# Kernel optimization log

Hardware: AMD Instinct MI355X
Metric: run time of the kernel (lower is better)

Reference implementation:

```python
import jax, jax.numpy as jnp
import numpy as np

T, D = 4096, 1024
S = 32768
DIST_DIM = 20
BINS = jnp.array([1, 2, 3, 4, 8, 16, 32, 64], dtype=jnp.int64)


def setup_inputs() -> dict:
    key = jax.random.key(0)
    ks = jax.random.split(key, 16)
    scale = 1.0 / np.sqrt(D)
    inp = {
        "embeds": jax.random.normal(ks[0], (T, D), dtype=jnp.float32),
        "states": jax.random.normal(ks[1], (T, D), dtype=jnp.float32),
        # MHA (1 head) projection params, torch Linear convention: x @ W.T + b
        "Wq": jax.random.normal(ks[2], (D, D), dtype=jnp.float32) * scale,
        "bq": jnp.zeros((D,), dtype=jnp.float32),
        "Wk": jax.random.normal(ks[3], (D, D), dtype=jnp.float32) * scale,
        "bk": jnp.zeros((D,), dtype=jnp.float32),
        "Wv": jax.random.normal(ks[4], (D, D), dtype=jnp.float32) * scale,
        "bv": jnp.zeros((D,), dtype=jnp.float32),
        "Wo": jax.random.normal(ks[5], (D, D), dtype=jnp.float32) * scale,
        "bo": jnp.zeros((D,), dtype=jnp.float32),
        # distance embedding table: len(bins)+1 = 9 rows
        "dist_embed": jax.random.normal(ks[6], (9, DIST_DIM), dtype=jnp.float32),
        "span_starts": jax.random.randint(ks[7], (S,), 0, T - 30, dtype=jnp.int64),
        "span_lengths": jax.random.randint(ks[8], (S,), 0, 30, dtype=jnp.int64),
    }
    return inp


def reference(embeds, states, Wq, bq, Wk, bk, Wv, bv, Wo, bo, dist_embed,
              span_starts, span_lengths):
    d = states.shape[1]
    # Single-head attention: query=states, key=states, value=embeds (seq len T, batch 1)
    q = states @ Wq.T + bq                      # [T, D]
    k = states @ Wk.T + bk                      # [T, D]
    v = embeds @ Wv.T + bv                      # [T, D]
    scores = (q @ k.T) / jnp.sqrt(jnp.asarray(d, q.dtype))   # [T, T]
    attn = jax.nn.softmax(scores, axis=-1)
    attn_embeds = (attn @ v) @ Wo.T + bo        # [T, D]

    ends = span_starts + span_lengths           # inclusive end, width 1..30
    # ragged per-span segment sum over [start, end] via prefix sums
    cs = jnp.concatenate([jnp.zeros((1, d), attn_embeds.dtype),
                          jnp.cumsum(attn_embeds, axis=0)], axis=0)  # [T+1, D]
    span_sum = cs[ends + 1] - cs[span_starts]   # [S, D]

    span_start_end = jnp.concatenate([states[span_starts], states[ends]], axis=1)  # [S, 2D]

    lengths = span_lengths + 1                  # len(span) = end - start + 1
    bin_idx = jnp.sum(lengths[:, None] > BINS[None, :], axis=-1)  # [S] in [0, 8]
    len_embed = dist_embed[bin_idx]             # [S, DIST_DIM] (dropout omitted: eval mode)

    return jnp.concatenate([span_sum, span_start_end, len_embed], axis=1)  # [S, 3D+20]
```

## Files before the change

kernel.cpp:

```cpp
#include <hip/hip_runtime.h>
#include <hip/hip_bf16.h>


typedef __attribute__((ext_vector_type(8))) short bf16x8;
typedef __attribute__((ext_vector_type(4))) short bf16x4;
typedef __attribute__((ext_vector_type(4))) float f32x4;

#define T_DIM 4096
#define D_DIM 1024
#define S_NUM 32768

#define GLOBAL_LOAD_LDS16(gptr, ldsptr)                                        \
  __builtin_amdgcn_global_load_lds(                                            \
      (const __attribute__((address_space(1))) void*)(gptr),                   \
      (__attribute__((address_space(3))) void*)(ldsptr), 16, 0, 0)

__global__ __launch_bounds__(256) void cast2_bf16(const float* __restrict__ a,
                                                  const float* __restrict__ b,
                                                  __hip_bfloat16* __restrict__ oa,
                                                  __hip_bfloat16* __restrict__ ob) {
  const float* s = blockIdx.z ? b : a;
  __hip_bfloat16* d = blockIdx.z ? ob : oa;
  int i = blockIdx.x * 256 + threadIdx.x;
  float2 v = ((const float2*)s)[i];
  __hip_bfloat162 o;
  o.x = __float2bfloat16(v.x);
  o.y = __float2bfloat16(v.y);
  ((__hip_bfloat162*)d)[i] = o;
}

__global__ __launch_bounds__(256) void cast1_bf16(const float* __restrict__ a,
                                                  __hip_bfloat16* __restrict__ oa) {
  int i = blockIdx.x * 256 + threadIdx.x;
  float2 v = ((const float2*)a)[i];
  __hip_bfloat162 o;
  o.x = __float2bfloat16(v.x);
  o.y = __float2bfloat16(v.y);
  ((__hip_bfloat162*)oa)[i] = o;
}

__global__ __launch_bounds__(256) void transpose_cast_bf16(const float* __restrict__ wq,
                                                           const float* __restrict__ wk,
                                                           const float* __restrict__ wv,
                                                           __hip_bfloat16* __restrict__ oq,
                                                           __hip_bfloat16* __restrict__ ok,
                                                           __hip_bfloat16* __restrict__ ov) {
  __shared__ float tile[64][65];
  const int z = blockIdx.z;
  const float* in = z == 0 ? wq : z == 1 ? wk : wv;
  __hip_bfloat16* out = z == 0 ? oq : z == 1 ? ok : ov;
  const int bx = blockIdx.x * 64;
  const int by = blockIdx.y * 64;
  const int t = threadIdx.x;
  const int r = t >> 4;
  const int c4 = (t & 15) * 4;
#pragma unroll
  for (int p = 0; p < 4; p++) {
    const float4 v = *(const float4*)&in[(size_t)(by + p * 16 + r) * D_DIM + bx + c4];
    tile[p * 16 + r][c4] = v.x;
    tile[p * 16 + r][c4 + 1] = v.y;
    tile[p * 16 + r][c4 + 2] = v.z;
    tile[p * 16 + r][c4 + 3] = v.w;
  }
  __syncthreads();
#pragma unroll
  for (int p = 0; p < 4; p++) {
    const int orow = p * 16 + r;
    bf16x4 o4;
#pragma unroll
    for (int q = 0; q < 4; q++) {
      __hip_bfloat16 h = __float2bfloat16(tile[c4 + q][orow]);
      o4[q] = *reinterpret_cast<short*>(&h);
    }
    *reinterpret_cast<bf16x4*>(&out[(size_t)(bx + orow) * D_DIM + by + c4]) = o4;
  }
}

__global__ __launch_bounds__(256) void zero_f32(float* __restrict__ p, int n) {
  int i = blockIdx.x * 256 + threadIdx.x;
  if (i < n) p[i] = 0.0f;
}

__global__ __launch_bounds__(256) void hvec(const float* __restrict__ Wo,
                                            const float* __restrict__ bv,
                                            const float* __restrict__ bo,
                                            const __hip_bfloat16* __restrict__ WqT,
                                            const __hip_bfloat16* __restrict__ WkT,
                                            const float* __restrict__ bq,
                                            const float* __restrict__ bk,
                                            float* __restrict__ bvo,
                                            float* __restrict__ h1,
                                            float* __restrict__ h2,
                                            float* __restrict__ c0) {
  const int z = blockIdx.z;
  const int wave = threadIdx.x >> 6, lane = threadIdx.x & 63;
  const int row = blockIdx.x * 4 + wave;
  if (z == 3 && (blockIdx.x != 0 || wave != 0)) return;
  float s = 0.0f;
  if (z == 0) {
    for (int k2 = lane; k2 < D_DIM; k2 += 64) s += Wo[(size_t)row * D_DIM + k2] * bv[k2];
  } else if (z == 1) {
    for (int k2 = lane; k2 < D_DIM; k2 += 64)
      s += __bfloat162float(WqT[(size_t)row * D_DIM + k2]) * bk[k2];
  } else if (z == 2) {
    for (int k2 = lane; k2 < D_DIM; k2 += 64)
      s += __bfloat162float(WkT[(size_t)row * D_DIM + k2]) * bq[k2];
  } else {
    for (int k2 = lane; k2 < D_DIM; k2 += 64) s += bq[k2] * bk[k2];
  }
#pragma unroll
  for (int off = 32; off; off >>= 1) s += __shfl_xor(s, off);
  if (lane == 0) {
    if (z == 0) bvo[row] = s + bo[row];
    else if (z == 1) h1[row] = s;
    else if (z == 2) h2[row] = s;
    else c0[0] = s;
  }
}

__global__ __launch_bounds__(256) void uw_vec(const float* __restrict__ states,
                                              const float* __restrict__ h1,
                                              const float* __restrict__ h2,
                                              const float* __restrict__ c0,
                                              float* __restrict__ u,
                                              float* __restrict__ w) {
  const int z = blockIdx.z;
  const int wave = threadIdx.x >> 6, lane = threadIdx.x & 63;
  const int row = blockIdx.x * 4 + wave;
  const float* h = z == 0 ? h1 : h2;
  float s = 0.0f;
  for (int k2 = lane; k2 < D_DIM; k2 += 64) s += states[(size_t)row * D_DIM + k2] * h[k2];
#pragma unroll
  for (int off = 32; off; off >>= 1) s += __shfl_xor(s, off);
  if (lane == 0) {
    if (z == 0) u[row] = s + c0[0];
    else w[row] = s;
  }
}

__device__ __forceinline__ void gemm_core_128(const __hip_bfloat16* __restrict__ A,
                                              const __hip_bfloat16* __restrict__ B,
                                              int K, int lda, int ldb,
                                              int bm, int bn,
                                              __hip_bfloat16* As,
                                              __hip_bfloat16* Bs,
                                              f32x4 acc[4][4]) {
  const int tid = threadIdx.x;
  const int wave = tid >> 6, lane = tid & 63;
  const int srow = lane >> 2, scol = (lane & 3) * 8;
  const __hip_bfloat16* Ag0 = A + (size_t)(bm + wave * 16 + srow) * lda + scol;
  const __hip_bfloat16* Ag1 = Ag0 + (size_t)64 * lda;
  const __hip_bfloat16* Bg0 = B + (size_t)(bn + wave * 16 + srow) * ldb + scol;
  const __hip_bfloat16* Bg1 = Bg0 + (size_t)64 * ldb;
  const int c0 = wave * 512, c1 = (4 + wave) * 512;
  const int wtr = (wave >> 1) * 64, wtc = (wave & 1) * 64;
  const int lr = lane & 15, lk = (lane >> 4) * 8;

  GLOBAL_LOAD_LDS16(Ag0, As + c0);
  GLOBAL_LOAD_LDS16(Ag1, As + c1);
  GLOBAL_LOAD_LDS16(Bg0, Bs + c0);
  GLOBAL_LOAD_LDS16(Bg1, Bs + c1);

  int cur = 0;
  for (int k0 = 0; k0 < K; k0 += 32) {
    __syncthreads();
    const int nxt = cur ^ 1;
    if (k0 + 32 < K) {
      const int kn = k0 + 32;
      GLOBAL_LOAD_LDS16(Ag0 + kn, As + nxt * 4096 + c0);
      GLOBAL_LOAD_LDS16(Ag1 + kn, As + nxt * 4096 + c1);
      GLOBAL_LOAD_LDS16(Bg0 + kn, Bs + nxt * 4096 + c0);
      GLOBAL_LOAD_LDS16(Bg1 + kn, Bs + nxt * 4096 + c1);
    }
    const __hip_bfloat16* a = As + cur * 4096;
    const __hip_bfloat16* b = Bs + cur * 4096;
    bf16x8 af[4], bfr[4];
#pragma unroll
    for (int i = 0; i < 4; i++)
      af[i] = *(const bf16x8*)&a[(wtr + i * 16 + lr) * 32 + lk];
#pragma unroll
    for (int j = 0; j < 4; j++)
      bfr[j] = *(const bf16x8*)&b[(wtc + j * 16 + lr) * 32 + lk];
#pragma unroll
    for (int i = 0; i < 4; i++)
#pragma unroll
      for (int j = 0; j < 4; j++)
        acc[i][j] = __builtin_amdgcn_mfma_f32_16x16x32_bf16(af[i], bfr[j], acc[i][j], 0, 0, 0);
    cur = nxt;
  }
}


__global__ __launch_bounds__(256) void small_gemm_splitk(const __hip_bfloat16* __restrict__ Wo_bf,
                                                         const __hip_bfloat16* __restrict__ WvT_bf,
                                                         const __hip_bfloat16* __restrict__ WkT_bf,
                                                         const __hip_bfloat16* __restrict__ WqT_bf,
                                                         float* __restrict__ part) {
  __shared__ __hip_bfloat16 As[2 * 128 * 32];
  __shared__ __hip_bfloat16 Bs[2 * 128 * 32];
  const int z = blockIdx.z;
  const int zz = z & 3;
  const __hip_bfloat16* A = (z < 4) ? Wo_bf + zz * 256 : WkT_bf + zz * 256;
  const __hip_bfloat16* B = (z < 4) ? WvT_bf + zz * 256 : WqT_bf + zz * 256;
  const int bm = blockIdx.y * 128, bn = blockIdx.x * 128;
  const int wave = threadIdx.x >> 6, lane = threadIdx.x & 63;
  const int wtr = (wave >> 1) * 64, wtc = (wave & 1) * 64;
  const int lr = lane & 15;
  f32x4 acc[4][4] = {};
  gemm_core_128(A, B, 256, D_DIM, D_DIM, bm, bn, As, Bs, acc);
  float* dst = part + (size_t)z * D_DIM * D_DIM;
#pragma unroll
  for (int j = 0; j < 4; j++) {
    const int col = bn + wtc + j * 16 + lr;
#pragma unroll
    for (int i = 0; i < 4; i++)
#pragma unroll
      for (int r = 0; r < 4; r++) {
        const int row = bm + wtr + i * 16 + (lane >> 4) * 4 + r;
        dst[(size_t)row * D_DIM + col] = acc[i][j][r];
      }
  }
}

__global__ __launch_bounds__(256) void small_combine(const float* __restrict__ part,
                                                     __hip_bfloat16* __restrict__ wvo,
                                                     __hip_bfloat16* __restrict__ m1) {
  const size_t idx = (size_t)blockIdx.x * 256 + threadIdx.x;
  const size_t n = (size_t)D_DIM * D_DIM / 4;
  const f32x4* base = (const f32x4*)part + (size_t)blockIdx.z * 4 * n;
  f32x4 s = base[idx] + base[idx + n] + base[idx + 2 * n] + base[idx + 3 * n];
  bf16x4 o;
#pragma unroll
  for (int q = 0; q < 4; q++) {
    __hip_bfloat16 h = __float2bfloat16(s[q]);
    o[q] = *reinterpret_cast<short*>(&h);
  }
  __hip_bfloat16* out = blockIdx.z == 0 ? wvo : m1;
  ((bf16x4*)out)[idx] = o;
}

__global__ __launch_bounds__(256) void proj_gemm(const __hip_bfloat16* __restrict__ states_bf,
                                                 const __hip_bfloat16* __restrict__ embeds_bf,
                                                 const __hip_bfloat16* __restrict__ M1,
                                                 const __hip_bfloat16* __restrict__ Wvo,
                                                 __hip_bfloat16* __restrict__ tmp,
                                                 __hip_bfloat16* __restrict__ vT) {
  __shared__ __hip_bfloat16 As[2 * 128 * 32];
  __shared__ __hip_bfloat16 Bs[2 * 128 * 32];
  const int z = blockIdx.z;
  const __hip_bfloat16* A = (z == 0) ? states_bf : embeds_bf;
  const __hip_bfloat16* B = (z == 0) ? M1 : Wvo;
  const int bm = blockIdx.y * 128, bn = blockIdx.x * 128;
  const int wave = threadIdx.x >> 6, lane = threadIdx.x & 63;
  const int wtr = (wave >> 1) * 64, wtc = (wave & 1) * 64;
  const int lr = lane & 15;
  f32x4 acc[4][4] = {};
  gemm_core_128(A, B, D_DIM, D_DIM, D_DIM, bm, bn, As, Bs, acc);

#pragma unroll
  for (int j = 0; j < 4; j++) {
    const int col = bn + wtc + j * 16 + lr;
#pragma unroll
    for (int i = 0; i < 4; i++) {
#pragma unroll
      for (int r = 0; r < 4; r++) {
        const int row = bm + wtr + i * 16 + (lane >> 4) * 4 + r;
        const __hip_bfloat16 val = __float2bfloat16(acc[i][j][r]);
        if (z == 0)
          tmp[(size_t)row * D_DIM + col] = val;
        else
          vT[(size_t)col * T_DIM + row] = val;
      }
    }
  }
}

__global__ __launch_bounds__(256) void scoresP_gemm(const __hip_bfloat16* __restrict__ tmp,
                                                    const __hip_bfloat16* __restrict__ states_bf,
                                                    const float* __restrict__ u,
                                                    const float* __restrict__ w,
                                                    __hip_bfloat16* __restrict__ P,
                                                    float* __restrict__ l) {
  __shared__ __hip_bfloat16 As[2 * 128 * 32];
  __shared__ __hip_bfloat16 Bs[2 * 128 * 32];
  const int bm = blockIdx.y * 128, bn = blockIdx.x * 128;
  const int wave = threadIdx.x >> 6, lane = threadIdx.x & 63;
  const int wtr = (wave >> 1) * 64, wtc = (wave & 1) * 64;
  const int lr = lane & 15;
  f32x4 acc[4][4] = {};
  gemm_core_128(tmp, states_bf, D_DIM, D_DIM, D_DIM, bm, bn, As, Bs, acc);

  float rowsum[4][4];
#pragma unroll
  for (int i = 0; i < 4; i++)
#pragma unroll
    for (int r = 0; r < 4; r++) rowsum[i][r] = 0.0f;

#pragma unroll
  for (int j = 0; j < 4; j++) {
    const int col = bn + wtc + j * 16 + lr;
    const float ww = w[col];
#pragma unroll
    for (int i = 0; i < 4; i++) {
#pragma unroll
      for (int r = 0; r < 4; r++) {
        const int row = bm + wtr + i * 16 + (lane >> 4) * 4 + r;
        const float e = __expf((acc[i][j][r] + u[row] + ww) * 0.03125f);
        P[(size_t)row * T_DIM + col] = __float2bfloat16(e);
        rowsum[i][r] += e;
      }
    }
  }
#pragma unroll
  for (int off = 1; off < 16; off <<= 1)
#pragma unroll
    for (int i = 0; i < 4; i++)
#pragma unroll
      for (int r = 0; r < 4; r++)
        rowsum[i][r] += __shfl_xor(rowsum[i][r], off);
  if ((lane & 15) == 0) {
#pragma unroll
    for (int i = 0; i < 4; i++)
#pragma unroll
      for (int r = 0; r < 4; r++) {
        const int row = bm + wtr + i * 16 + (lane >> 4) * 4 + r;
        atomicAdd(&l[row], rowsum[i][r]);
      }
  }
}

__global__ __launch_bounds__(256) void pv_gemm_splitk(const __hip_bfloat16* __restrict__ P,
                                                      const __hip_bfloat16* __restrict__ vT,
                                                      float* __restrict__ part) {
  __shared__ __hip_bfloat16 As[2 * 128 * 32];
  __shared__ __hip_bfloat16 Bs[2 * 128 * 32];
  const int z = blockIdx.z;
  const int bm = blockIdx.y * 128, bn = blockIdx.x * 128;
  const int wave = threadIdx.x >> 6, lane = threadIdx.x & 63;
  const int wtr = (wave >> 1) * 64, wtc = (wave & 1) * 64;
  const int lr = lane & 15;
  f32x4 acc[4][4] = {};
  gemm_core_128(P + z * 2048, vT + z * 2048, 2048, T_DIM, T_DIM, bm, bn, As, Bs, acc);
  float* dst = part + (size_t)z * T_DIM * D_DIM;
#pragma unroll
  for (int j = 0; j < 4; j++) {
    const int col = bn + wtc + j * 16 + lr;
#pragma unroll
    for (int i = 0; i < 4; i++)
#pragma unroll
      for (int r = 0; r < 4; r++) {
        const int row = bm + wtr + i * 16 + (lane >> 4) * 4 + r;
        dst[(size_t)row * D_DIM + col] = acc[i][j][r];
      }
  }
}

__global__ __launch_bounds__(256) void pv_combine_colsum(const float* __restrict__ part,
                                                         const float* __restrict__ l,
                                                         const float* __restrict__ bvo,
                                                         float* __restrict__ ao,
                                                         float* __restrict__ partT) {
  const int col = blockIdx.x * 256 + threadIdx.x;
  const int ch = blockIdx.y;
  const size_t n = (size_t)T_DIM * D_DIM;
  const float bb = bvo[col];
  float s = 0.0f;
  for (int i = 0; i < 64; i++) {
    const int row = ch * 64 + i;
    const float inv = 1.0f / l[row];
    const size_t idx = (size_t)row * D_DIM + col;
    const float v = (part[idx] + part[n + idx]) * inv + bb;
    ao[idx] = v;
    s += v;
  }
  partT[(col << 6) | ch] = s;
}

__global__ __launch_bounds__(256) void write_cs(const float* __restrict__ x,
                                                const float* __restrict__ partT,
                                                float* __restrict__ cs) {
  const int col = blockIdx.x * 256 + threadIdx.x;
  const int ch = blockIdx.y;
  float run = 0.0f;
  for (int c = 0; c < ch; c++) run += partT[(col << 6) | c];
  if (ch == 0) cs[col] = 0.0f;
  const float* p = x + (size_t)ch * 64 * D_DIM + col;
  float* q = cs + ((size_t)(ch * 64 + 1)) * D_DIM + col;
  for (int i = 0; i < 64; i++) {
    run += p[i * D_DIM];
    q[i * D_DIM] = run;
  }
}

__global__ __launch_bounds__(256) void hist_k(const int* __restrict__ starts,
                                              int* __restrict__ hist) {
  const int s = blockIdx.x * 256 + threadIdx.x;
  atomicAdd(&hist[starts[s]], 1);
}

__global__ __launch_bounds__(1024) void scan_hist(const int* __restrict__ hist,
                                                  int* __restrict__ offs) {
  __shared__ int sums[1024];
  const int t = threadIdx.x;
  const int v0 = hist[t * 4], v1 = hist[t * 4 + 1];
  const int v2 = hist[t * 4 + 2], v3 = hist[t * 4 + 3];
  const int tot = v0 + v1 + v2 + v3;
  sums[t] = tot;
  __syncthreads();
  for (int off = 1; off < 1024; off <<= 1) {
    const int x = (t >= off) ? sums[t - off] : 0;
    __syncthreads();
    sums[t] += x;
    __syncthreads();
  }
  const int excl = sums[t] - tot;
  offs[t * 4] = excl;
  offs[t * 4 + 1] = excl + v0;
  offs[t * 4 + 2] = excl + v0 + v1;
  offs[t * 4 + 3] = excl + v0 + v1 + v2;
}

__global__ __launch_bounds__(256) void scatter_k(const int* __restrict__ starts,
                                                 int* __restrict__ offs,
                                                 int* __restrict__ perm) {
  const int s = blockIdx.x * 256 + threadIdx.x;
  const int pos = atomicAdd(&offs[starts[s]], 1);
  perm[pos] = s;
}

__global__ __launch_bounds__(256) void span_gather(const float* __restrict__ cs,
                                                   const float* __restrict__ states,
                                                   const float* __restrict__ dist,
                                                   const int* __restrict__ starts,
                                                   const int* __restrict__ lens,
                                                   const int* __restrict__ perm,
                                                   float* __restrict__ out) {
  const int s = perm[blockIdx.x];
  const int start = starts[s];
  const int len = lens[s];
  const int end = start + len;
  const int length = len + 1;
  const int bin = (length > 1) + (length > 2) + (length > 3) + (length > 4) +
                  (length > 8) + (length > 16) + (length > 32) + (length > 64);
  const f32x4* csS = (const f32x4*)(cs + (size_t)start * D_DIM);
  const f32x4* csE = (const f32x4*)(cs + (size_t)(end + 1) * D_DIM);
  const f32x4* stS = (const f32x4*)(states + (size_t)start * D_DIM);
  const f32x4* stE = (const f32x4*)(states + (size_t)end * D_DIM);
  const f32x4* de = (const f32x4*)(dist + bin * 20);
  f32x4* o = (f32x4*)(out + (size_t)s * 3092);
  for (int j = threadIdx.x; j < 773; j += 256) {
    f32x4 r;
    if (j < 256) {
      r = csE[j] - csS[j];
    } else if (j < 512) {
      r = stS[j - 256];
    } else if (j < 768) {
      r = stE[j - 512];
    } else {
      r = de[j - 768];
    }
    __builtin_nontemporal_store(r, o + j);
  }
}

extern "C" void kernel_launch(void* const* d_in, const int* in_sizes, int n_in,
                              void* d_out, int out_size, void* d_ws, size_t ws_size,
                              hipStream_t stream) {
  const float* embeds = (const float*)d_in[0];
  const float* states = (const float*)d_in[1];
  const float* Wq = (const float*)d_in[2];
  const float* bq = (const float*)d_in[3];
  const float* Wk = (const float*)d_in[4];
  const float* bk = (const float*)d_in[5];
  const float* Wv = (const float*)d_in[6];
  const float* bv = (const float*)d_in[7];
  const float* Wo = (const float*)d_in[8];
  const float* bo = (const float*)d_in[9];
  const float* dist = (const float*)d_in[10];
  const int* starts = (const int*)d_in[11];
  const int* lens = (const int*)d_in[12];
  float* out = (float*)d_out;

  const size_t TD = (size_t)T_DIM * D_DIM;
  const size_t DD = (size_t)D_DIM * D_DIM;
  const size_t TT = (size_t)T_DIM * T_DIM;

  char* w = (char*)d_ws;
  size_t off = 0;
  auto alloc = [&](size_t bytes) {
    char* p = w + off;
    off = (off + bytes + 255) & ~(size_t)255;
    return p;
  };
  __hip_bfloat16* states_bf = (__hip_bfloat16*)alloc(TD * 2);
  __hip_bfloat16* embeds_bf = (__hip_bfloat16*)alloc(TD * 2);
  __hip_bfloat16* Wo_bf = (__hip_bfloat16*)alloc(DD * 2);
  __hip_bfloat16* WqT_bf = (__hip_bfloat16*)alloc(DD * 2);
  __hip_bfloat16* WkT_bf = (__hip_bfloat16*)alloc(DD * 2);
  __hip_bfloat16* WvT_bf = (__hip_bfloat16*)alloc(DD * 2);
  __hip_bfloat16* Wvo_bf = (__hip_bfloat16*)alloc(DD * 2);
  __hip_bfloat16* M1_bf = (__hip_bfloat16*)alloc(DD * 2);
  __hip_bfloat16* tmp_bf = (__hip_bfloat16*)alloc(TD * 2);
  __hip_bfloat16* vT_bf = (__hip_bfloat16*)alloc(TD * 2);
  __hip_bfloat16* P_bf = (__hip_bfloat16*)alloc(TT * 2);
  float* l_sum = (float*)alloc(T_DIM * 4);
  int* hist = (int*)alloc(T_DIM * 4);
  int* offs = (int*)alloc(T_DIM * 4);
  int* perm = (int*)alloc(S_NUM * 4);
  float* bvo = (float*)alloc(D_DIM * 4);
  float* h1 = (float*)alloc(D_DIM * 4);
  float* h2 = (float*)alloc(D_DIM * 4);
  float* c0 = (float*)alloc(256);
  float* u = (float*)alloc(T_DIM * 4);
  float* wv_ = (float*)alloc(T_DIM * 4);
  float* ao = (float*)alloc(TD * 4);
  float* cs = (float*)alloc((size_t)(T_DIM + 1) * D_DIM * 4);
  float* partT = (float*)alloc(64 * D_DIM * 4);
  float* wpart = (float*)alloc(8 * DD * 4);
  float* pv_part = (float*)alloc(2 * TD * 4);
  if (off > ws_size) return;

  cast2_bf16<<<dim3(TD / 512, 1, 2), 256, 0, stream>>>(states, embeds, states_bf, embeds_bf);
  cast1_bf16<<<DD / 512, 256, 0, stream>>>(Wo, Wo_bf);
  transpose_cast_bf16<<<dim3(16, 16, 3), 256, 0, stream>>>(Wq, Wk, Wv, WqT_bf, WkT_bf, WvT_bf);
  zero_f32<<<2 * T_DIM / 256, 256, 0, stream>>>(l_sum, 2 * T_DIM);
  hvec<<<dim3(D_DIM / 4, 1, 4), 256, 0, stream>>>(Wo, bv, bo, WqT_bf, WkT_bf, bq, bk,
                                                  bvo, h1, h2, c0);

  hist_k<<<S_NUM / 256, 256, 0, stream>>>(starts, hist);
  scan_hist<<<1, 1024, 0, stream>>>(hist, offs);
  scatter_k<<<S_NUM / 256, 256, 0, stream>>>(starts, offs, perm);

  uw_vec<<<dim3(T_DIM / 4, 1, 2), 256, 0, stream>>>(states, h1, h2, c0, u, wv_);

  small_gemm_splitk<<<dim3(D_DIM / 128, D_DIM / 128, 8), 256, 0, stream>>>(
      Wo_bf, WvT_bf, WkT_bf, WqT_bf, wpart);
  small_combine<<<dim3(DD / 1024, 1, 2), 256, 0, stream>>>(wpart, Wvo_bf, M1_bf);

  proj_gemm<<<dim3(D_DIM / 128, T_DIM / 128, 2), 256, 0, stream>>>(
      states_bf, embeds_bf, M1_bf, Wvo_bf, tmp_bf, vT_bf);

  scoresP_gemm<<<dim3(T_DIM / 128, T_DIM / 128), 256, 0, stream>>>(
      tmp_bf, states_bf, u, wv_, P_bf, l_sum);

  pv_gemm_splitk<<<dim3(D_DIM / 128, T_DIM / 128, 2), 256, 0, stream>>>(P_bf, vT_bf, pv_part);
  pv_combine_colsum<<<dim3(4, 64), 256, 0, stream>>>(pv_part, l_sum, bvo, ao, partT);

  write_cs<<<dim3(4, 64), 256, 0, stream>>>(ao, partT, cs);

  span_gather<<<S_NUM, 256, 0, stream>>>(cs, states, dist, starts, lens, perm, out);
}
```

Baseline: 725.9 us.

## Replace split-K PV GEMM with 128x64 tiles and fused normalize/colsum epilogue

Drops split-K in the P·V GEMM and shrinks the N tile to 64 so the grid keeps the same block count, giving each block the full K range. The softmax normalization, bias add, ao write and per-64-row column partial sums now happen in the GEMM epilogue via wave shuffles. This removes the separate combine kernel and the write and read of two fp32 T×D partial buffers. The cost is a longer K loop per block and less B-tile reuse per A load.

Measured after the change: 726.6 us. About the same (+0.1%).

```diff
diff --git a/kernel.cpp b/kernel.cpp
--- a/kernel.cpp
+++ b/kernel.cpp
@@ -190,6 +190,55 @@
   }
 }
 
+__device__ __forceinline__ void gemm_core_128x64(const __hip_bfloat16* __restrict__ A,
+                                                 const __hip_bfloat16* __restrict__ B,
+                                                 int K, int lda, int ldb,
+                                                 int bm, int bn,
+                                                 __hip_bfloat16* As,
+                                                 __hip_bfloat16* Bs,
+                                                 f32x4 acc[4][2]) {
+  const int tid = threadIdx.x;
+  const int wave = tid >> 6, lane = tid & 63;
+  const int srow = lane >> 2, scol = (lane & 3) * 8;
+  const __hip_bfloat16* Ag0 = A + (size_t)(bm + wave * 16 + srow) * lda + scol;
+  const __hip_bfloat16* Ag1 = Ag0 + (size_t)64 * lda;
+  const __hip_bfloat16* Bg0 = B + (size_t)(bn + wave * 16 + srow) * ldb + scol;
+  const int c0 = wave * 512, c1 = (4 + wave) * 512;
+  const int wtr = (wave >> 1) * 64, wtc = (wave & 1) * 32;
+  const int lr = lane & 15, lk = (lane >> 4) * 8;
+
+  GLOBAL_LOAD_LDS16(Ag0, As + c0);
+  GLOBAL_LOAD_LDS16(Ag1, As + c1);
+  GLOBAL_LOAD_LDS16(Bg0, Bs + c0);
+
+  int cur = 0;
+  for (int k0 = 0; k0 < K; k0 += 32) {
+    __syncthreads();
+    const int nxt = cur ^ 1;
+    if (k0 + 32 < K) {
+      const int kn = k0 + 32;
+      GLOBAL_LOAD_LDS16(Ag0 + kn, As + nxt * 4096 + c0);
+      GLOBAL_LOAD_LDS16(Ag1 + kn, As + nxt * 4096 + c1);
+      GLOBAL_LOAD_LDS16(Bg0 + kn, Bs + nxt * 2048 + c0);
+    }
+    const __hip_bfloat16* a = As + cur * 4096;
+    const __hip_bfloat16* b = Bs + cur * 2048;
+    bf16x8 af[4], bfr[2];
+#pragma unroll
+    for (int i = 0; i < 4; i++)
+      af[i] = *(const bf16x8*)&a[(wtr + i * 16 + lr) * 32 + lk];
+#pragma unroll
+    for (int j = 0; j < 2; j++)
+      bfr[j] = *(const bf16x8*)&b[(wtc + j * 16 + lr) * 32 + lk];
+#pragma unroll
+    for (int i = 0; i < 4; i++)
+#pragma unroll
+      for (int j = 0; j < 2; j++)
+        acc[i][j] = __builtin_amdgcn_mfma_f32_16x16x32_bf16(af[i], bfr[j], acc[i][j], 0, 0, 0);
+    cur = nxt;
+  }
+}
+
 
 __global__ __launch_bounds__(256) void small_gemm_splitk(const __hip_bfloat16* __restrict__ Wo_bf,
                                                          const __hip_bfloat16* __restrict__ WvT_bf,
@@ -329,51 +378,59 @@
   }
 }
 
-__global__ __launch_bounds__(256) void pv_gemm_splitk(const __hip_bfloat16* __restrict__ P,
-                                                      const __hip_bfloat16* __restrict__ vT,
-                                                      float* __restrict__ part) {
+__global__ __launch_bounds__(256) void pv_gemm(const __hip_bfloat16* __restrict__ P,
+                                               const __hip_bfloat16* __restrict__ vT,
+                                               const float* __restrict__ l,
+                                               const float* __restrict__ bvo,
+                                               float* __restrict__ ao,
+                                               float* __restrict__ partT) {
   __shared__ __hip_bfloat16 As[2 * 128 * 32];
-  __shared__ __hip_bfloat16 Bs[2 * 128 * 32];
-  const int z = blockIdx.z;
-  const int bm = blockIdx.y * 128, bn = blockIdx.x * 128;
+  __shared__ __hip_bfloat16 Bs[2 * 64 * 32];
+  const int bm = blockIdx.y * 128, bn = blockIdx.x * 64;
   const int wave = threadIdx.x >> 6, lane = threadIdx.x & 63;
-  const int wtr = (wave >> 1) * 64, wtc = (wave & 1) * 64;
+  const int wtr = (wave >> 1) * 64, wtc = (wave & 1) * 32;
   const int lr = lane & 15;
-  f32x4 acc[4][4] = {};
-  gemm_core_128(P + z * 2048, vT + z * 2048, 2048, T_DIM, T_DIM, bm, bn, As, Bs, acc);
-  float* dst = part + (size_t)z * T_DIM * D_DIM;
-#pragma unroll
-  for (int j = 0; j < 4; j++) {
+  f32x4 acc[4][2] = {};
+  gemm_core_128x64(P, vT, T_DIM, T_DIM, T_DIM, bm, bn, As, Bs, acc);
+
+  float inv[4][4];
+#pragma unroll
+  for (int i = 0; i < 4; i++)
+#pragma unroll
+    for (int r = 0; r < 4; r++) {
+      const int row = bm + wtr + i * 16 + (lane >> 4) * 4 + r;
+      inv[i][r] = 1.0f / l[row];
+    }
+  const int ch = (bm >> 6) + (wave >> 1);
+  float csum[2];
+#pragma unroll
+  for (int j = 0; j < 2; j++) {
     const int col = bn + wtc + j * 16 + lr;
+    const float bb = bvo[col];
+    float s = 0.0f;
 #pragma unroll
     for (int i = 0; i < 4; i++)
 #pragma unroll
       for (int r = 0; r < 4; r++) {
         const int row = bm + wtr + i * 16 + (lane >> 4) * 4 + r;
-        dst[(size_t)row * D_DIM + col] = acc[i][j][r];
+        const float v = acc[i][j][r] * inv[i][r] + bb;
+        ao[(size_t)row * D_DIM + col] = v;
+        s += v;
       }
-  }
-}
-
-__global__ __launch_bounds__(256) void pv_combine_colsum(const float* __restrict__ part,
-                                                         const float* __restrict__ l,
-                                                         const float* __restrict__ bvo,
-                                                         float* __restrict__ ao,
-                                                         float* __restrict__ partT) {
-  const int col = blockIdx.x * 256 + threadIdx.x;
-  const int ch = blockIdx.y;
-  const size_t n = (size_t)T_DIM * D_DIM;
-  const float bb = bvo[col];
-  float s = 0.0f;
-  for (int i = 0; i < 64; i++) {
-    const int row = ch * 64 + i;
-    const float inv = 1.0f / l[row];
-    const size_t idx = (size_t)row * D_DIM + col;
-    const float v = (part[idx] + part[n + idx]) * inv + bb;
-    ao[idx] = v;
-    s += v;
-  }
-  partT[(col << 6) | ch] = s;
+    csum[j] = s;
+  }
+#pragma unroll
+  for (int j = 0; j < 2; j++) {
+    csum[j] += __shfl_xor(csum[j], 16);
+    csum[j] += __shfl_xor(csum[j], 32);
+  }
+  if (lane < 16) {
+#pragma unroll
+    for (int j = 0; j < 2; j++) {
+      const int col = bn + wtc + j * 16 + lane;
+      partT[(col << 6) | ch] = csum[j];
+    }
+  }
 }
 
 __global__ __launch_bounds__(256) void write_cs(const float* __restrict__ x,
@@ -517,7 +574,6 @@
   float* cs = (float*)alloc((size_t)(T_DIM + 1) * D_DIM * 4);
   float* partT = (float*)alloc(64 * D_DIM * 4);
   float* wpart = (float*)alloc(8 * DD * 4);
-  float* pv_part = (float*)alloc(2 * TD * 4);
   if (off > ws_size) return;
 
   cast2_bf16<<<dim3(TD / 512, 1, 2), 256, 0, stream>>>(states, embeds, states_bf, embeds_bf);
@@ -543,8 +599,8 @@
   scoresP_gemm<<<dim3(T_DIM / 128, T_DIM / 128), 256, 0, stream>>>(
       tmp_bf, states_bf, u, wv_, P_bf, l_sum);
 
-  pv_gemm_splitk<<<dim3(D_DIM / 128, T_DIM / 128, 2), 256, 0, stream>>>(P_bf, vT_bf, pv_part);
-  pv_combine_colsum<<<dim3(4, 64), 256, 0, stream>>>(pv_part, l_sum, bvo, ao, partT);
+  pv_gemm<<<dim3(D_DIM / 64, T_DIM / 128), 256, 0, stream>>>(
+      P_bf, vT_bf, l_sum, bvo, ao, partT);
 
   write_cs<<<dim3(4, 64), 256, 0, stream>>>(ao, partT, cs);
 
```
